# Performance work log

Hardware: AMD Instinct MI355X
Metric: run time of the kernel (lower is better)

## Reference

```python
import jax, jax.numpy as jnp
import numpy as np

N, F_IN, E = 20000, 256, 320000
H, C = 8, 128            # conv1 heads, per-head channels
OUT, DH = 1, 128         # output_dim, dense_hidden
G = 64                   # number of graphs
EPS = 1e-5


def setup_inputs() -> dict:
    key = jax.random.key(0)
    ks = jax.random.split(key, 20)
    s = 0.05
    return {
        'x': jax.random.normal(ks[0], (N, F_IN), jnp.float32),
        'edge_index': jax.random.randint(ks[1], (2, E), 0, N, jnp.int64),
        'batch': jnp.sort(jax.random.randint(ks[2], (N,), 0, G, jnp.int64)),
        # conv1 (GATv2, heads=8, concat)
        'w1_l': jax.random.normal(ks[3], (F_IN, H * C), jnp.float32) * s,
        'w1_r': jax.random.normal(ks[4], (F_IN, H * C), jnp.float32) * s,
        'att1': jax.random.normal(ks[5], (H, C), jnp.float32) * s,
        'b1': jnp.zeros((H * C,), jnp.float32),
        # norm1 (BatchNorm over H*C features)
        'g1': jnp.ones((H * C,), jnp.float32),
        'be1': jnp.zeros((H * C,), jnp.float32),
        # conv2 (GATv2, heads=1, concat=False)
        'w2_l': jax.random.normal(ks[6], (H * C, OUT), jnp.float32) * s,
        'w2_r': jax.random.normal(ks[7], (H * C, OUT), jnp.float32) * s,
        'att2': jax.random.normal(ks[8], (1, OUT), jnp.float32) * s,
        'b2': jnp.zeros((OUT,), jnp.float32),
        # norm2
        'g2': jnp.ones((OUT,), jnp.float32),
        'be2': jnp.zeros((OUT,), jnp.float32),
        # MLP head
        'lw1': jax.random.normal(ks[9], (OUT, DH), jnp.float32) * s,
        'lb1': jnp.zeros((DH,), jnp.float32),
        'lw2': jax.random.normal(ks[10], (DH, OUT), jnp.float32) * s,
        'lb2': jnp.zeros((OUT,), jnp.float32),
    }


def gatv2(x, src, dst, wl, wr, att, bias, heads, ch, concat):
    n = x.shape[0]
    xl = (x @ wl).reshape(n, heads, ch)
    xr = (x @ wr).reshape(n, heads, ch)
    # edge-wise GATv2 score: a^T LeakyReLU(x_l[j] + x_r[i]), slope 0.2
    e = jnp.einsum('ehc,hc->eh', jax.nn.leaky_relu(xl[src] + xr[dst], 0.2), att)
    # segment softmax over incoming edges per target node
    emax = jax.ops.segment_max(e, dst, num_segments=n)
    ee = jnp.exp(e - emax[dst])
    denom = jax.ops.segment_sum(ee, dst, num_segments=n)
    alpha = ee / (denom[dst] + 1e-16)
    out = jax.ops.segment_sum(alpha[..., None] * xl[src], dst, num_segments=n)  # [n,h,c]
    if concat:
        return out.reshape(n, heads * ch) + bias
    return out.mean(axis=1) + bias


def batchnorm(x, g, b):
    mu = x.mean(axis=0)
    var = ((x - mu) ** 2).mean(axis=0)
    return (x - mu) * jax.lax.rsqrt(var + EPS) * g + b


def reference(x, edge_index, batch, w1_l, w1_r, att1, b1, g1, be1,
              w2_l, w2_r, att2, b2, g2, be2, lw1, lb1, lw2, lb2):
    n = x.shape[0]
    loops = jnp.arange(n, dtype=edge_index.dtype)
    src = jnp.concatenate([edge_index[0], loops])  # add self-loops (PyG default)
    dst = jnp.concatenate([edge_index[1], loops])

    h = gatv2(x, src, dst, w1_l, w1_r, att1, b1, H, C, concat=True)
    h = jax.nn.leaky_relu(batchnorm(h, g1, be1), 0.01)
    # dropout: eval mode (identity)
    h = gatv2(h, src, dst, w2_l, w2_r, att2, b2, 1, OUT, concat=False)
    h = jax.nn.leaky_relu(batchnorm(h, g2, be2), 0.01)

    # global mean pool over graphs
    sums = jax.ops.segment_sum(h, batch, num_segments=G)
    cnt = jax.ops.segment_sum(jnp.ones((n, 1), h.dtype), batch, num_segments=G)
    pooled = sums / jnp.maximum(cnt, 1.0)

    out = jax.nn.leaky_relu(pooled @ lw1 + lb1, 0.01)
    return out @ lw2 + lb2
```

## Files before the change

### kernel.cpp

```cpp
#include <hip/hip_runtime.h>
#include <hip/hip_bf16.h>


__device__ __forceinline__ float lrelu(float x, float s) { return x > 0.f ? x : s * x; }

typedef _Float16 half8 __attribute__((ext_vector_type(8)));
typedef _Float16 half4v __attribute__((ext_vector_type(4)));
typedef _Float16 half2v __attribute__((ext_vector_type(2)));
typedef float f32x4 __attribute__((ext_vector_type(4)));

#define GLOBAL_AS __attribute__((address_space(1)))
#define LDS_AS __attribute__((address_space(3)))

__device__ __forceinline__ void async_copy16(const void* g, void* l) {
  __builtin_amdgcn_global_load_lds((const GLOBAL_AS unsigned int*)g,
                                   (LDS_AS unsigned int*)l, 16, 0, 0);
}

__global__ void zero_ints(int* __restrict__ p, int n) {
  const int t = blockIdx.x * blockDim.x + threadIdx.x;
  if (t < n) p[t] = 0;
}

__global__ void edge_hist(const int* __restrict__ ei, int E, int N,
                          int* __restrict__ counts) {
  const int t = blockIdx.x * blockDim.x + threadIdx.x;
  if (t >= E + N) return;
  const int dst = (t < E) ? ei[E + t] : (t - E);
  atomicAdd(&counts[dst], 1);
}

__global__ __launch_bounds__(1024) void scan_counts(const int* __restrict__ counts,
                                                    int* __restrict__ row_ptr,
                                                    int* __restrict__ cursor, int N) {
  __shared__ int sdata[1024];
  __shared__ int lcnt[20480];
  const int t = threadIdx.x;
  if (N <= 20480) {
    for (int j = t; j < N; j += 1024) lcnt[j] = counts[j];
    __syncthreads();
    const int chunk = (N + 1023) / 1024;
    const int s0 = min(N, t * chunk);
    const int s1 = min(N, s0 + chunk);
    int lsum = 0;
    for (int i = s0; i < s1; ++i) lsum += lcnt[i];
    sdata[t] = lsum;
    __syncthreads();
    for (int off = 1; off < 1024; off <<= 1) {
      int v = 0;
      if (t >= off) v = sdata[t - off];
      __syncthreads();
      sdata[t] += v;
      __syncthreads();
    }
    int run = sdata[t] - lsum;
    for (int i = s0; i < s1; ++i) { const int c = lcnt[i]; lcnt[i] = run; run += c; }
    if (s0 < N && s1 == N) row_ptr[N] = run;
    __syncthreads();
    for (int j = t; j < N; j += 1024) {
      const int v = lcnt[j];
      row_ptr[j] = v;
      cursor[j] = v;
    }
  } else {
    const int chunk = (N + 1023) / 1024;
    const int s0 = min(N, t * chunk);
    const int s1 = min(N, s0 + chunk);
    int lsum = 0;
    for (int i = s0; i < s1; ++i) lsum += counts[i];
    sdata[t] = lsum;
    __syncthreads();
    for (int off = 1; off < 1024; off <<= 1) {
      int v = 0;
      if (t >= off) v = sdata[t - off];
      __syncthreads();
      sdata[t] += v;
      __syncthreads();
    }
    int run = sdata[t] - lsum;
    for (int i = s0; i < s1; ++i) {
      row_ptr[i] = run;
      cursor[i] = run;
      run += counts[i];
    }
    if (s0 < N && s1 == N) row_ptr[N] = run;
  }
}

__global__ void edge_scatter(const int* __restrict__ ei, int E, int N,
                             int* __restrict__ cursor, int* __restrict__ col) {
  const int t = blockIdx.x * blockDim.x + threadIdx.x;
  if (t >= E + N) return;
  const int dst = (t < E) ? ei[E + t] : (t - E);
  const int src = (t < E) ? ei[t] : (t - E);
  const int pos = atomicAdd(&cursor[dst], 1);
  col[pos] = src;
}

__global__ void convert_x(const float* __restrict__ x, _Float16* __restrict__ A2, int M) {
  const int t = blockIdx.x * blockDim.x + threadIdx.x;
  if (t >= M * 64) return;
  const int m = t >> 6;
  const int k4 = (t & 63) * 4;
  const float4 v = *(const float4*)(x + (size_t)m * 256 + k4);
  const float sx = 16.f;
  *(half4v*)(A2 + (size_t)m * 256 + k4) =
      (half4v){(_Float16)(v.x * sx), (_Float16)(v.y * sx),
               (_Float16)(v.z * sx), (_Float16)(v.w * sx)};
}

__global__ __launch_bounds__(256) void convert_w(const float* __restrict__ wl,
                                                 const float* __restrict__ wr,
                                                 _Float16* __restrict__ B2,
                                                 int colOff, int W) {
  const int n = blockIdx.x;
  const int k = threadIdx.x;
  const float v = 16.f * ((n < W) ? wl[k * 1024 + colOff + n]
                                  : wr[k * 1024 + colOff + (n - W)]);
  B2[(size_t)n * 256 + k] = (_Float16)v;
}

__global__ __launch_bounds__(256) void gemm_mfma(const _Float16* __restrict__ A2,
                                                 const _Float16* __restrict__ B2,
                                                 _Float16* __restrict__ C,
                                                 int M, int Ntot) {
  __shared__ __align__(16) _Float16 LDSbuf[2 * 128 * 64];
  _Float16* As = LDSbuf;
  _Float16* Bs = LDSbuf + 128 * 64;
  const int tid = threadIdx.x;
  const int lane = tid & 63;
  const int wv = tid >> 6;
  const int wm = wv & 1, wn = wv >> 1;
  const int m_blk = blockIdx.y * 128;
  const int n_blk = blockIdx.x * 128;
  const int row16 = lane & 15, quad = lane >> 4;
  f32x4 acc[4][4] = {};

  for (int kt = 0; kt < 4; ++kt) {
    const int kg = kt * 64;
#pragma unroll
    for (int j = 0; j < 4; ++j) {
      const int ci = j * 256 + tid;
      const int row = ci >> 3;
      const int c = ci & 7;
      const int gc = c ^ (row & 7);
      _Float16* ldsA = &As[(j * 256 + wv * 64) * 8];
      _Float16* ldsB = &Bs[(j * 256 + wv * 64) * 8];
      const int growA = min(m_blk + row, M - 1);
      async_copy16(A2 + (size_t)growA * 256 + kg + gc * 8, ldsA);
      async_copy16(B2 + (size_t)(n_blk + row) * 256 + kg + gc * 8, ldsB);
    }
    __syncthreads();
#pragma unroll
    for (int ks = 0; ks < 2; ++ks) {
      half8 af[4], bf[4];
#pragma unroll
      for (int mi = 0; mi < 4; ++mi) {
        const int r = wm * 64 + mi * 16 + row16;
        const int cl = (ks * 4 + quad) ^ (r & 7);
        af[mi] = *(const half8*)&As[r * 64 + cl * 8];
      }
#pragma unroll
      for (int ni = 0; ni < 4; ++ni) {
        const int r = wn * 64 + ni * 16 + row16;
        const int cl = (ks * 4 + quad) ^ (r & 7);
        bf[ni] = *(const half8*)&Bs[r * 64 + cl * 8];
      }
#pragma unroll
      for (int mi = 0; mi < 4; ++mi)
#pragma unroll
        for (int ni = 0; ni < 4; ++ni)
          acc[mi][ni] = __builtin_amdgcn_mfma_f32_16x16x32_f16(af[mi], bf[ni], acc[mi][ni], 0, 0, 0);
    }
    __syncthreads();
  }
  const float inv = 1.f / 256.f;
  _Float16* tw = LDSbuf + wv * 4096;
#pragma unroll
  for (int mi = 0; mi < 4; ++mi)
#pragma unroll
    for (int reg = 0; reg < 4; ++reg) {
      const int r_in = mi * 16 + quad * 4 + reg;
#pragma unroll
      for (int ni = 0; ni < 4; ++ni)
        tw[r_in * 64 + ni * 16 + row16] = (_Float16)(acc[mi][ni][reg] * inv);
    }
#pragma unroll
  for (int p8 = 0; p8 < 8; ++p8) {
    const int row = p8 * 8 + (lane >> 3);
    const int grow = m_blk + wm * 64 + row;
    if (grow < M) {
      const half8 v = *(const half8*)&tw[row * 64 + (lane & 7) * 8];
      *(half8*)(C + (size_t)grow * Ntot + n_blk + wn * 64 + (lane & 7) * 8) = v;
    }
  }
}

__global__ __launch_bounds__(256, 8) void conv1_attn_hw(const _Float16* __restrict__ xlrp,
                                                        const int* __restrict__ row_ptr,
                                                        const int* __restrict__ col,
                                                        const float* __restrict__ att,
                                                        const float* __restrict__ bias,
                                                        _Float16* __restrict__ h1, int N) {
  union H8 { half8 v; half2v p[4]; };
  const int wv = threadIdx.x >> 6;
  const int lane = threadIdx.x & 63;
  const int i = blockIdx.x * 2 + (wv >> 1);
  if (i >= N) return;
  const int f = (wv & 1) * 512 + lane * 8;
  half2v a2[4], xr2[4];
  float acc[8];
#pragma unroll
  for (int p = 0; p < 4; ++p)
    a2[p] = (half2v){(_Float16)att[f + 2 * p], (_Float16)att[f + 2 * p + 1]};
  {
    H8 u;
    u.v = *(const half8*)(xlrp + (size_t)i * 2048 + 1024 + f);
#pragma unroll
    for (int k = 0; k < 4; ++k) xr2[k] = u.p[k];
  }
#pragma unroll
  for (int c = 0; c < 8; ++c) acc[c] = 0.f;
  float m = -3.0e38f, l = 0.f;
  const int kb = row_ptr[i];
  const int ke = row_ptr[i + 1];
  for (int base = kb; base < ke; base += 64) {
    const int cnt = min(64, ke - base);
    const int myc = (lane < cnt) ? col[base + lane] : 0;
    H8 xc, xn;
    {
      const int s0 = __shfl(myc, 0);
      xc.v = *(const half8*)(xlrp + (size_t)s0 * 2048 + f);
    }
    for (int q = 0; q < cnt; ++q) {
      if (q + 1 < cnt) {
        const int sn = __shfl(myc, q + 1);
        xn.v = *(const half8*)(xlrp + (size_t)sn * 2048 + f);
      }
      float s = 0.f;
#pragma unroll
      for (int p = 0; p < 4; ++p) {
        const half2v xp = xc.p[p];
        const half2v t = xp + xr2[p];
        const half2v t5 = t * (half2v){(_Float16)0.2f, (_Float16)0.2f};
        const half2v lr = __builtin_elementwise_max(t, t5);
        s = __builtin_amdgcn_fdot2(a2[p], lr, s, false);
      }
      s += __shfl_xor(s, 8);
      s += __shfl_xor(s, 4);
      s += __shfl_xor(s, 2);
      s += __shfl_xor(s, 1);
      if (s <= m) {
        const float pw = __expf(s - m);
        l += pw;
#pragma unroll
        for (int p = 0; p < 4; ++p) {
          const half2v xp = xc.p[p];
          acc[2 * p] += pw * (float)xp[0];
          acc[2 * p + 1] += pw * (float)xp[1];
        }
      } else {
        const float sc = __expf(m - s);
        m = s;
        l = l * sc + 1.f;
#pragma unroll
        for (int p = 0; p < 4; ++p) {
          const half2v xp = xc.p[p];
          acc[2 * p] = acc[2 * p] * sc + (float)xp[0];
          acc[2 * p + 1] = acc[2 * p + 1] * sc + (float)xp[1];
        }
      }
      xc = xn;
    }
  }
  const float inv = 1.f / (l + 1e-16f);
  H8 u;
#pragma unroll
  for (int k = 0; k < 4; ++k) {
    const int c = 2 * k;
    u.p[k] = (half2v){(_Float16)(acc[c] * inv + bias[f + c]),
                      (_Float16)(acc[c + 1] * inv + bias[f + c + 1])};
  }
  *(half8*)(h1 + (size_t)i * 1024 + f) = u.v;
}

template <int CPT>
__global__ __launch_bounds__(256, 6) void conv1_attn(const _Float16* __restrict__ xlrp,
                                                     const int* __restrict__ row_ptr,
                                                     const int* __restrict__ col,
                                                     const float* __restrict__ att,
                                                     const float* __restrict__ bias,
                                                     _Float16* __restrict__ h1,
                                                     int W, int N) {
  constexpr int PAIRS = CPT / 2;
  constexpr int NV8 = CPT / 8;
  constexpr int HG = 128 / CPT;
  union H8 { half8 v; half2v p[4]; };
  const int lane = threadIdx.x & 63;
  const int i = blockIdx.x * 4 + (threadIdx.x >> 6);
  if (i >= N) return;
  const int f = lane * CPT;
  half2v a2[PAIRS], xr2[PAIRS];
  float acc[CPT];
#pragma unroll
  for (int p = 0; p < PAIRS; ++p)
    a2[p] = (half2v){(_Float16)att[f + 2 * p], (_Float16)att[f + 2 * p + 1]};
  {
    const half8* xrp = (const half8*)(xlrp + (size_t)i * (2 * W) + W + f);
#pragma unroll
    for (int j = 0; j < NV8; ++j) {
      H8 u; u.v = xrp[j];
#pragma unroll
      for (int k = 0; k < 4; ++k) xr2[j * 4 + k] = u.p[k];
    }
  }
#pragma unroll
  for (int c = 0; c < CPT; ++c) acc[c] = 0.f;
  float m = -3.0e38f, l = 0.f;
  const int kb = row_ptr[i];
  const int ke = row_ptr[i + 1];
  for (int base = kb; base < ke; base += 64) {
    const int cnt = min(64, ke - base);
    const int myc = (lane < cnt) ? col[base + lane] : 0;
    H8 xc[NV8], xn[NV8];
    {
      const int s0 = __shfl(myc, 0);
      const half8* rp = (const half8*)(xlrp + (size_t)s0 * (2 * W) + f);
#pragma unroll
      for (int j = 0; j < NV8; ++j) xc[j].v = rp[j];
    }
    for (int q = 0; q < cnt; ++q) {
      if (q + 1 < cnt) {
        const int sn = __shfl(myc, q + 1);
        const half8* rp = (const half8*)(xlrp + (size_t)sn * (2 * W) + f);
#pragma unroll
        for (int j = 0; j < NV8; ++j) xn[j].v = rp[j];
      }
      float s = 0.f;
#pragma unroll
      for (int p = 0; p < PAIRS; ++p) {
        const half2v xp = xc[p >> 2].p[p & 3];
        const half2v t = xp + xr2[p];
        const half2v t5 = t * (half2v){(_Float16)0.2f, (_Float16)0.2f};
        const half2v lr = __builtin_elementwise_max(t, t5);
        s = __builtin_amdgcn_fdot2(a2[p], lr, s, false);
      }
#pragma unroll
      for (int off = HG / 2; off >= 1; off >>= 1) s += __shfl_xor(s, off);
      if (s <= m) {
        const float pw = __expf(s - m);
        l += pw;
#pragma unroll
        for (int p = 0; p < PAIRS; ++p) {
          const half2v xp = xc[p >> 2].p[p & 3];
          acc[2 * p] += pw * (float)xp[0];
          acc[2 * p + 1] += pw * (float)xp[1];
        }
      } else {
        const float sc = __expf(m - s);
        m = s;
        l = l * sc + 1.f;
#pragma unroll
        for (int p = 0; p < PAIRS; ++p) {
          const half2v xp = xc[p >> 2].p[p & 3];
          acc[2 * p] = acc[2 * p] * sc + (float)xp[0];
          acc[2 * p + 1] = acc[2 * p + 1] * sc + (float)xp[1];
        }
      }
#pragma unroll
      for (int j = 0; j < NV8; ++j) xc[j] = xn[j];
    }
  }
  const float inv = 1.f / (l + 1e-16f);
  _Float16* outp = h1 + (size_t)i * 1024 + f;
#pragma unroll
  for (int j = 0; j < NV8; ++j) {
    H8 u;
#pragma unroll
    for (int k = 0; k < 4; ++k) {
      const int c = j * 8 + 2 * k;
      u.p[k] = (half2v){(_Float16)(acc[c] * inv + bias[f + c]),
                        (_Float16)(acc[c + 1] * inv + bias[f + c + 1])};
    }
    ((half8*)outp)[j] = u.v;
  }
}

__global__ __launch_bounds__(256) void bn1_stats(const _Float16* __restrict__ h1,
                                                 float* __restrict__ bsum,
                                                 float* __restrict__ bsq, int N) {
  const int f = threadIdx.x * 4;
  const int chunk = (N + 255) / 256;
  const int r0 = blockIdx.y * chunk;
  const int r1 = min(N, r0 + chunk);
  float s0 = 0.f, s1 = 0.f, s2 = 0.f, s3 = 0.f;
  float q0 = 0.f, q1 = 0.f, q2 = 0.f, q3 = 0.f;
  for (int r = r0; r < r1; ++r) {
    const half4v v4 = *(const half4v*)(h1 + (size_t)r * 1024 + f);
    const float v0 = (float)v4[0], v1 = (float)v4[1], v2 = (float)v4[2], v3 = (float)v4[3];
    s0 += v0; q0 += v0 * v0;
    s1 += v1; q1 += v1 * v1;
    s2 += v2; q2 += v2 * v2;
    s3 += v3; q3 += v3 * v3;
  }
  atomicAdd(&bsum[f + 0], s0); atomicAdd(&bsq[f + 0], q0);
  atomicAdd(&bsum[f + 1], s1); atomicAdd(&bsq[f + 1], q1);
  atomicAdd(&bsum[f + 2], s2); atomicAdd(&bsq[f + 2], q2);
  atomicAdd(&bsum[f + 3], s3); atomicAdd(&bsq[f + 3], q3);
}

__global__ __launch_bounds__(256) void bn1_proj(const _Float16* __restrict__ h1,
                                                const float* __restrict__ bsum,
                                                const float* __restrict__ bsq,
                                                const float* __restrict__ g1,
                                                const float* __restrict__ be1,
                                                const float* __restrict__ w2l,
                                                const float* __restrict__ w2r,
                                                float* __restrict__ xl2,
                                                float* __restrict__ xr2, int N) {
  const int i = blockIdx.x;
  const int tid = threadIdx.x;
  const int f = tid * 4;
  const half4v hv = *(const half4v*)(h1 + (size_t)i * 1024 + f);
  const float4 h4 = make_float4((float)hv[0], (float)hv[1], (float)hv[2], (float)hv[3]);
  const float4 s4 = *(const float4*)(bsum + f);
  const float4 q4 = *(const float4*)(bsq + f);
  const float4 g4 = *(const float4*)(g1 + f);
  const float4 b4 = *(const float4*)(be1 + f);
  const float4 wl = *(const float4*)(w2l + f);
  const float4 wr = *(const float4*)(w2r + f);
  const float invN = 1.f / (float)N;
  float pl = 0.f, pr = 0.f;
  {
    float mu, var, rs, v;
    mu = s4.x * invN; var = q4.x * invN - mu * mu; rs = 1.f / sqrtf(var + 1e-5f);
    v = lrelu((h4.x - mu) * rs * g4.x + b4.x, 0.01f); pl += v * wl.x; pr += v * wr.x;
    mu = s4.y * invN; var = q4.y * invN - mu * mu; rs = 1.f / sqrtf(var + 1e-5f);
    v = lrelu((h4.y - mu) * rs * g4.y + b4.y, 0.01f); pl += v * wl.y; pr += v * wr.y;
    mu = s4.z * invN; var = q4.z * invN - mu * mu; rs = 1.f / sqrtf(var + 1e-5f);
    v = lrelu((h4.z - mu) * rs * g4.z + b4.z, 0.01f); pl += v * wl.z; pr += v * wr.z;
    mu = s4.w * invN; var = q4.w * invN - mu * mu; rs = 1.f / sqrtf(var + 1e-5f);
    v = lrelu((h4.w - mu) * rs * g4.w + b4.w, 0.01f); pl += v * wl.w; pr += v * wr.w;
  }
#pragma unroll
  for (int off = 32; off; off >>= 1) {
    pl += __shfl_down(pl, off);
    pr += __shfl_down(pr, off);
  }
  __shared__ float sp[8];
  if ((tid & 63) == 0) {
    sp[tid >> 6] = pl;
    sp[4 + (tid >> 6)] = pr;
  }
  __syncthreads();
  if (tid == 0) {
    xl2[i] = sp[0] + sp[1] + sp[2] + sp[3];
    xr2[i] = sp[4] + sp[5] + sp[6] + sp[7];
  }
}

__global__ __launch_bounds__(256) void conv2_attn(const float* __restrict__ xl2,
                                                  const float* __restrict__ xr2,
                                                  const int* __restrict__ row_ptr,
                                                  const int* __restrict__ col,
                                                  const float* __restrict__ att2,
                                                  const float* __restrict__ b2,
                                                  float* __restrict__ out2,
                                                  float* __restrict__ bn2acc, int N) {
  const int i = blockIdx.x * blockDim.x + threadIdx.x;
  float val = 0.f;
  if (i < N) {
    const float a = att2[0];
    const float xr = xr2[i];
    float m = -3.0e38f, l = 0.f, acc = 0.f;
    const int kb = row_ptr[i];
    const int ke = row_ptr[i + 1];
    for (int k = kb; k < ke; ++k) {
      const float xv = xl2[col[k]];
      const float s = a * lrelu(xv + xr, 0.2f);
      const float mn = fmaxf(m, s);
      const float sc = __expf(m - mn);
      const float p = __expf(s - mn);
      l = l * sc + p;
      acc = acc * sc + p * xv;
      m = mn;
    }
    val = acc / (l + 1e-16f) + b2[0];
    out2[i] = val;
  }
  float s = (i < N) ? val : 0.f;
  float q = s * s;
#pragma unroll
  for (int off = 32; off; off >>= 1) {
    s += __shfl_down(s, off);
    q += __shfl_down(q, off);
  }
  __shared__ float red[8];
  if ((threadIdx.x & 63) == 0) {
    red[threadIdx.x >> 6] = s;
    red[4 + (threadIdx.x >> 6)] = q;
  }
  __syncthreads();
  if (threadIdx.x == 0) {
    atomicAdd(&bn2acc[0], red[0] + red[1] + red[2] + red[3]);
    atomicAdd(&bn2acc[1], red[4] + red[5] + red[6] + red[7]);
  }
}

__global__ __launch_bounds__(256) void bn2_pool(const float* __restrict__ out2,
                                                const float* __restrict__ bn2acc,
                                                const float* __restrict__ g2,
                                                const float* __restrict__ be2,
                                                const int* __restrict__ batch,
                                                float* __restrict__ pool_sum,
                                                float* __restrict__ pool_cnt, int N) {
  __shared__ float ls[64];
  __shared__ float lc[64];
  const int tid = threadIdx.x;
  if (tid < 64) { ls[tid] = 0.f; lc[tid] = 0.f; }
  __syncthreads();
  const int i = blockIdx.x * blockDim.x + tid;
  if (i < N) {
    const float invN = 1.f / (float)N;
    const float mu = bn2acc[0] * invN;
    const float var = bn2acc[1] * invN - mu * mu;
    const float rs = 1.f / sqrtf(var + 1e-5f);
    const float v = lrelu((out2[i] - mu) * rs * g2[0] + be2[0], 0.01f);
    const int g = batch[i];
    atomicAdd(&ls[g], v);
    atomicAdd(&lc[g], 1.f);
  }
  __syncthreads();
  if (tid < 64 && lc[tid] != 0.f) {
    atomicAdd(&pool_sum[tid], ls[tid]);
    atomicAdd(&pool_cnt[tid], lc[tid]);
  }
}

__global__ void head_mlp(const float* __restrict__ pool_sum, const float* __restrict__ pool_cnt,
                         const float* __restrict__ lw1, const float* __restrict__ lb1,
                         const float* __restrict__ lw2, const float* __restrict__ lb2,
                         float* __restrict__ out) {
  const int g = threadIdx.x;
  if (g >= 64) return;
  const float p = pool_sum[g] / fmaxf(pool_cnt[g], 1.f);
  float acc = 0.f;
  for (int d = 0; d < 128; ++d) {
    float t = p * lw1[d] + lb1[d];
    t = lrelu(t, 0.01f);
    acc += t * lw2[d];
  }
  out[g] = acc + lb2[0];
}

extern "C" void kernel_launch(void* const* d_in, const int* in_sizes, int n_in,
                              void* d_out, int out_size, void* d_ws, size_t ws_size,
                              hipStream_t stream) {
  const float* x = (const float*)d_in[0];
  const int* ei = (const int*)d_in[1];
  const int* batch = (const int*)d_in[2];
  const float* w1_l = (const float*)d_in[3];
  const float* w1_r = (const float*)d_in[4];
  const float* att1 = (const float*)d_in[5];
  const float* b1 = (const float*)d_in[6];
  const float* g1 = (const float*)d_in[7];
  const float* be1 = (const float*)d_in[8];
  const float* w2_l = (const float*)d_in[9];
  const float* w2_r = (const float*)d_in[10];
  const float* att2 = (const float*)d_in[11];
  const float* b2 = (const float*)d_in[12];
  const float* g2 = (const float*)d_in[13];
  const float* be2 = (const float*)d_in[14];
  const float* lw1 = (const float*)d_in[15];
  const float* lb1 = (const float*)d_in[16];
  const float* lw2 = (const float*)d_in[17];
  const float* lb2 = (const float*)d_in[18];

  const int N = in_sizes[2];
  const int E = in_sizes[1] / 2;
  const int ET = E + N;

  const size_t AL = 255;
  auto al = [&](size_t b) { return (b + AL) & ~AL; };
  const size_t zbytes = (size_t)N * 4 + 4096 + 4096 + 16 + 256 + 256;
  const size_t fixedNoXlr = al((size_t)N * 2048)
                          + 3 * al((size_t)N * 4)
                          + al((size_t)(N + 1) * 4)
                          + al((size_t)ET * 4)
                          + al((size_t)N * 4)
                          + al(zbytes);
  const size_t a2b = al((size_t)N * 256 * 2);
  int P = 1;
  while (P < 8) {
    const size_t xlrb = al((size_t)N * (4096 / P));
    const size_t b2b = al((size_t)(2 * (1024 / P)) * 256 * 2);
    const size_t extra = (P == 1) ? 0 : (a2b + b2b);
    if (fixedNoXlr + xlrb + extra <= ws_size) break;
    P <<= 1;
  }
  const int W = 1024 / P;

  char* ws = (char*)d_ws;
  size_t off = 0;
  auto alloc = [&](size_t b) { size_t p = off; off += al(b); return p; };
  _Float16* h1 = (_Float16*)(ws + alloc((size_t)N * 2048));
  _Float16* xlrp = (_Float16*)(ws + alloc((size_t)N * (4096 / P)));
  float* xl2 = (float*)(ws + alloc((size_t)N * 4));
  float* xr2 = (float*)(ws + alloc((size_t)N * 4));
  float* out2 = (float*)(ws + alloc((size_t)N * 4));
  int* row_ptr = (int*)(ws + alloc((size_t)(N + 1) * 4));
  int* colb = (int*)(ws + alloc((size_t)ET * 4));
  int* cursor = (int*)(ws + alloc((size_t)N * 4));
  char* zbase = ws + alloc(zbytes);
  int* counts = (int*)zbase;
  float* bn1_sum = (float*)(zbase + (size_t)N * 4);
  float* bn1_sq = (float*)(zbase + (size_t)N * 4 + 4096);
  float* bn2acc = (float*)(zbase + (size_t)N * 4 + 8192);
  float* pool_sum = (float*)(zbase + (size_t)N * 4 + 8192 + 16);
  float* pool_cnt = (float*)(zbase + (size_t)N * 4 + 8192 + 16 + 256);

  _Float16 *A2, *B2;
  if (P == 1) {
    A2 = (_Float16*)h1;
    B2 = (_Float16*)((char*)h1 + a2b);
  } else {
    A2 = (_Float16*)(ws + alloc((size_t)N * 256 * 2));
    B2 = (_Float16*)(ws + alloc((size_t)(2 * W) * 256 * 2));
  }

  const int zn = (int)(zbytes / 4);
  zero_ints<<<(zn + 255) / 256, 256, 0, stream>>>((int*)zbase, zn);

  edge_hist<<<(ET + 255) / 256, 256, 0, stream>>>(ei, E, N, counts);
  scan_counts<<<1, 1024, 0, stream>>>(counts, row_ptr, cursor, N);
  edge_scatter<<<(ET + 255) / 256, 256, 0, stream>>>(ei, E, N, cursor, colb);

  convert_x<<<(N * 64 + 255) / 256, 256, 0, stream>>>(x, A2, N);
  for (int p = 0; p < P; ++p) {
    convert_w<<<2 * W, 256, 0, stream>>>(w1_l, w1_r, B2, p * W, W);
    gemm_mfma<<<dim3(2 * W / 128, (N + 127) / 128), 256, 0, stream>>>(A2, B2, xlrp, N, 2 * W);
    if (W >= 1024)
      conv1_attn_hw<<<(N + 1) / 2, 256, 0, stream>>>(xlrp, row_ptr, colb,
                                                     att1, b1, h1, N);
    else
      conv1_attn<8><<<(N + 3) / 4, 256, 0, stream>>>(xlrp, row_ptr, colb,
                                                     att1 + p * W, b1 + p * W,
                                                     h1 + p * W, W, N);
  }

  bn1_stats<<<dim3(1, 256), 256, 0, stream>>>(h1, bn1_sum, bn1_sq, N);
  bn1_proj<<<N, 256, 0, stream>>>(h1, bn1_sum, bn1_sq, g1, be1, w2_l, w2_r, xl2, xr2, N);
  conv2_attn<<<(N + 255) / 256, 256, 0, stream>>>(xl2, xr2, row_ptr, colb, att2, b2,
                                                  out2, bn2acc, N);
  bn2_pool<<<(N + 255) / 256, 256, 0, stream>>>(out2, bn2acc, g2, be2, batch, pool_sum, pool_cnt, N);
  head_mlp<<<1, 64, 0, stream>>>(pool_sum, pool_cnt, lw1, lb1, lw2, lb2, (float*)d_out);
}
```

Baseline: 388.0 us.

## Replace BN1 atomics with per-chunk partials and precompute scale/shift

bn1_stats now writes per-chunk partial sums and squares to a buffer instead of using global atomics. A new bn1_final kernel reduces the partials and folds mean, variance, gamma and beta into one per-feature scale and shift. bn1_proj becomes a persistent kernel of 512 blocks that loops over rows and applies only an FMA per element. The aim is to remove atomic contention and repeated per-row rsqrt work. The trade-off is fewer stats blocks (64 instead of 256) to stream h1, plus a serialized per-row loop with two barriers per row, which may reduce memory parallelism.

```diff
diff --git a/kernel.cpp b/kernel.cpp
--- a/kernel.cpp
+++ b/kernel.cpp
@@ -387,11 +387,11 @@
 }
 
 __global__ __launch_bounds__(256) void bn1_stats(const _Float16* __restrict__ h1,
-                                                 float* __restrict__ bsum,
-                                                 float* __restrict__ bsq, int N) {
+                                                 float* __restrict__ part, int N) {
   const int f = threadIdx.x * 4;
-  const int chunk = (N + 255) / 256;
-  const int r0 = blockIdx.y * chunk;
+  const int y = blockIdx.y;
+  const int chunk = (N + 63) / 64;
+  const int r0 = y * chunk;
   const int r1 = min(N, r0 + chunk);
   float s0 = 0.f, s1 = 0.f, s2 = 0.f, s3 = 0.f;
   float q0 = 0.f, q1 = 0.f, q2 = 0.f, q3 = 0.f;
@@ -403,59 +403,74 @@
     s2 += v2; q2 += v2 * v2;
     s3 += v3; q3 += v3 * v3;
   }
-  atomicAdd(&bsum[f + 0], s0); atomicAdd(&bsq[f + 0], q0);
-  atomicAdd(&bsum[f + 1], s1); atomicAdd(&bsq[f + 1], q1);
-  atomicAdd(&bsum[f + 2], s2); atomicAdd(&bsq[f + 2], q2);
-  atomicAdd(&bsum[f + 3], s3); atomicAdd(&bsq[f + 3], q3);
+  float* ps = part + y * 1024 + f;
+  ps[0] = s0; ps[1] = s1; ps[2] = s2; ps[3] = s3;
+  float* pq = part + 65536 + y * 1024 + f;
+  pq[0] = q0; pq[1] = q1; pq[2] = q2; pq[3] = q3;
+}
+
+__global__ __launch_bounds__(256) void bn1_final(const float* __restrict__ part,
+                                                 const float* __restrict__ g1,
+                                                 const float* __restrict__ be1,
+                                                 float* __restrict__ scale1,
+                                                 float* __restrict__ shift1, int N) {
+  const int c = blockIdx.x * 256 + threadIdx.x;
+  float s = 0.f, q = 0.f;
+  for (int y = 0; y < 64; ++y) {
+    s += part[y * 1024 + c];
+    q += part[65536 + y * 1024 + c];
+  }
+  const float invN = 1.f / (float)N;
+  const float mu = s * invN;
+  const float var = q * invN - mu * mu;
+  const float rs = 1.f / sqrtf(var + 1e-5f);
+  const float sc = rs * g1[c];
+  scale1[c] = sc;
+  shift1[c] = be1[c] - mu * sc;
 }
 
 __global__ __launch_bounds__(256) void bn1_proj(const _Float16* __restrict__ h1,
-                                                const float* __restrict__ bsum,
-                                                const float* __restrict__ bsq,
-                                                const float* __restrict__ g1,
-                                                const float* __restrict__ be1,
+                                                const float* __restrict__ scale1,
+                                                const float* __restrict__ shift1,
                                                 const float* __restrict__ w2l,
                                                 const float* __restrict__ w2r,
                                                 float* __restrict__ xl2,
                                                 float* __restrict__ xr2, int N) {
-  const int i = blockIdx.x;
   const int tid = threadIdx.x;
   const int f = tid * 4;
-  const half4v hv = *(const half4v*)(h1 + (size_t)i * 1024 + f);
-  const float4 h4 = make_float4((float)hv[0], (float)hv[1], (float)hv[2], (float)hv[3]);
-  const float4 s4 = *(const float4*)(bsum + f);
-  const float4 q4 = *(const float4*)(bsq + f);
-  const float4 g4 = *(const float4*)(g1 + f);
-  const float4 b4 = *(const float4*)(be1 + f);
+  const float4 sc4 = *(const float4*)(scale1 + f);
+  const float4 sh4 = *(const float4*)(shift1 + f);
   const float4 wl = *(const float4*)(w2l + f);
   const float4 wr = *(const float4*)(w2r + f);
-  const float invN = 1.f / (float)N;
-  float pl = 0.f, pr = 0.f;
-  {
-    float mu, var, rs, v;
-    mu = s4.x * invN; var = q4.x * invN - mu * mu; rs = 1.f / sqrtf(var + 1e-5f);
-    v = lrelu((h4.x - mu) * rs * g4.x + b4.x, 0.01f); pl += v * wl.x; pr += v * wr.x;
-    mu = s4.y * invN; var = q4.y * invN - mu * mu; rs = 1.f / sqrtf(var + 1e-5f);
-    v = lrelu((h4.y - mu) * rs * g4.y + b4.y, 0.01f); pl += v * wl.y; pr += v * wr.y;
-    mu = s4.z * invN; var = q4.z * invN - mu * mu; rs = 1.f / sqrtf(var + 1e-5f);
-    v = lrelu((h4.z - mu) * rs * g4.z + b4.z, 0.01f); pl += v * wl.z; pr += v * wr.z;
-    mu = s4.w * invN; var = q4.w * invN - mu * mu; rs = 1.f / sqrtf(var + 1e-5f);
-    v = lrelu((h4.w - mu) * rs * g4.w + b4.w, 0.01f); pl += v * wl.w; pr += v * wr.w;
-  }
-#pragma unroll
-  for (int off = 32; off; off >>= 1) {
-    pl += __shfl_down(pl, off);
-    pr += __shfl_down(pr, off);
-  }
   __shared__ float sp[8];
-  if ((tid & 63) == 0) {
-    sp[tid >> 6] = pl;
-    sp[4 + (tid >> 6)] = pr;
-  }
-  __syncthreads();
-  if (tid == 0) {
-    xl2[i] = sp[0] + sp[1] + sp[2] + sp[3];
-    xr2[i] = sp[4] + sp[5] + sp[6] + sp[7];
+  const int per = (N + gridDim.x - 1) / gridDim.x;
+  const int i0 = blockIdx.x * per;
+  const int i1 = min(N, i0 + per);
+  for (int i = i0; i < i1; ++i) {
+    const half4v hv = *(const half4v*)(h1 + (size_t)i * 1024 + f);
+    float pl = 0.f, pr = 0.f;
+    {
+      float v;
+      v = lrelu((float)hv[0] * sc4.x + sh4.x, 0.01f); pl += v * wl.x; pr += v * wr.x;
+      v = lrelu((float)hv[1] * sc4.y + sh4.y, 0.01f); pl += v * wl.y; pr += v * wr.y;
+      v = lrelu((float)hv[2] * sc4.z + sh4.z, 0.01f); pl += v * wl.z; pr += v * wr.z;
+      v = lrelu((float)hv[3] * sc4.w + sh4.w, 0.01f); pl += v * wl.w; pr += v * wr.w;
+    }
+#pragma unroll
+    for (int off = 32; off; off >>= 1) {
+      pl += __shfl_down(pl, off);
+      pr += __shfl_down(pr, off);
+    }
+    if ((tid & 63) == 0) {
+      sp[tid >> 6] = pl;
+      sp[4 + (tid >> 6)] = pr;
+    }
+    __syncthreads();
+    if (tid == 0) {
+      xl2[i] = sp[0] + sp[1] + sp[2] + sp[3];
+      xr2[i] = sp[4] + sp[5] + sp[6] + sp[7];
+    }
+    __syncthreads();
   }
 }
 
@@ -588,7 +603,9 @@
                           + al((size_t)(N + 1) * 4)
                           + al((size_t)ET * 4)
                           + al((size_t)N * 4)
-                          + al(zbytes);
+                          + al(zbytes)
+                          + al(131072 * 4)
+                          + 2 * al(4096);
   const size_t a2b = al((size_t)N * 256 * 2);
   int P = 1;
   while (P < 8) {
@@ -613,11 +630,12 @@
   int* cursor = (int*)(ws + alloc((size_t)N * 4));
   char* zbase = ws + alloc(zbytes);
   int* counts = (int*)zbase;
-  float* bn1_sum = (float*)(zbase + (size_t)N * 4);
-  float* bn1_sq = (float*)(zbase + (size_t)N * 4 + 4096);
   float* bn2acc = (float*)(zbase + (size_t)N * 4 + 8192);
   float* pool_sum = (float*)(zbase + (size_t)N * 4 + 8192 + 16);
   float* pool_cnt = (float*)(zbase + (size_t)N * 4 + 8192 + 16 + 256);
+  float* bn1_part = (float*)(ws + alloc(131072 * 4));
+  float* bn1_scale = (float*)(ws + alloc(4096));
+  float* bn1_shift = (float*)(ws + alloc(4096));
 
   _Float16 *A2, *B2;
   if (P == 1) {
@@ -648,8 +666,9 @@
                                                      h1 + p * W, W, N);
   }
 
-  bn1_stats<<<dim3(1, 256), 256, 0, stream>>>(h1, bn1_sum, bn1_sq, N);
-  bn1_proj<<<N, 256, 0, stream>>>(h1, bn1_sum, bn1_sq, g1, be1, w2_l, w2_r, xl2, xr2, N);
+  bn1_stats<<<dim3(1, 64), 256, 0, stream>>>(h1, bn1_part, N);
+  bn1_final<<<4, 256, 0, stream>>>(bn1_part, g1, be1, bn1_scale, bn1_shift, N);
+  bn1_proj<<<512, 256, 0, stream>>>(h1, bn1_scale, bn1_shift, w2_l, w2_r, xl2, xr2, N);
   conv2_attn<<<(N + 255) / 256, 256, 0, stream>>>(xl2, xr2, row_ptr, colb, att2, b2,
                                                   out2, bn2acc, N);
   bn2_pool<<<(N + 255) / 256, 256, 0, stream>>>(out2, bn2acc, g2, be2, batch, pool_sum, pool_cnt, N);
```

Measured after the change: 428.8 us. 1.11x slower.
